# Kernel optimization log

Measured on AMD Instinct MI355X. Metric: run time of the kernel, lower is better.

Reference implementation:

```python
import jax, jax.numpy as jnp
import numpy as np


def blockdiag_matmul(x, w):
    """Block-diagonal (Monarch) linear: w has shape (nblocks, out_blk, in_blk);
    x has shape (..., nblocks*in_blk); returns (..., nblocks*out_blk)."""
    nb, q, p = w.shape
    lead = x.shape[:-1]
    xb = x.reshape(-1, nb, p)  # (tokens, nblocks, in_blk)
    out = jnp.einsum('bnp,nqp->bnq', xb, w)  # per-block matmul
    return out.reshape(*lead, nb * q)


def setup_inputs() -> dict:
    key = jax.random.key(0)
    k_x, k1, k2, k3 = jax.random.split(key, 4)
    B, S, D = 4, 4096, 2048
    NB, FF = 4, 8192  # nblocks, adjusted intermediate size
    # Kaiming-uniform-like scale for block weights (fan_in = D or FF per block-row)
    s1 = 1.0 / np.sqrt(D)
    s2 = 1.0 / np.sqrt(FF)
    return {
        'x': jax.random.normal(k_x, (B, S, D), dtype=jnp.float32),
        'w1': jax.random.normal(k1, (NB, FF // NB, D // NB), dtype=jnp.float32) * s1,
        'w3': jax.random.normal(k3, (NB, FF // NB, D // NB), dtype=jnp.float32) * s1,
        'w2': jax.random.normal(k2, (NB, D // NB, FF // NB), dtype=jnp.float32) * s2,
    }


def reference(x, w1, w3, w2):
    # SwiGLU MLP: w2(silu(w1(x)) * w3(x)), all projections block-diagonal
    gate = jax.nn.silu(blockdiag_matmul(x, w1))
    up = blockdiag_matmul(x, w3)
    return blockdiag_matmul(gate * up, w2)
```

## Files before the change

### kernel.cpp

```cpp
#include <hip/hip_runtime.h>
#include <cstdint>

typedef __attribute__((ext_vector_type(8))) short bf16x8;
typedef __attribute__((ext_vector_type(4))) float f32x4;
typedef unsigned short u16;

#define RD(p) (*(const bf16x8*)(p))

__device__ inline u16 f2bf(float f) {
  union { float f; unsigned int u; } v; v.f = f;
  unsigned int u = v.u;
  unsigned int r = (u + 0x7fffu + ((u >> 16) & 1u)) >> 16;
  return (u16)r;
}

__device__ inline void gload_lds16(const u16* g, u16* l) {
  __builtin_amdgcn_global_load_lds(
      (const __attribute__((address_space(1))) void*)g,
      (__attribute__((address_space(3))) void*)l, 16, 0, 0);
}

#define PH_BEGIN() \
  __builtin_amdgcn_s_barrier(); \
  asm volatile("s_waitcnt lgkmcnt(0)" ::: "memory"); \
  __builtin_amdgcn_s_setprio(1)
#define PH_END() \
  __builtin_amdgcn_s_setprio(0); \
  __builtin_amdgcn_s_barrier()

__global__ void cvt_all(const float* __restrict__ x, const float* __restrict__ w1,
                        const float* __restrict__ w3, const float* __restrict__ w2,
                        u16* __restrict__ xb, u16* __restrict__ w1b,
                        u16* __restrict__ w3b, u16* __restrict__ w2b) {
  const int nx = 4194304;
  const int nw = 524288;
  const int total = nx + 3 * nw;
  int stride = gridDim.x * blockDim.x;
  for (int i = blockIdx.x * blockDim.x + threadIdx.x; i < total; i += stride) {
    const float* src; u16* dst; int j;
    if (i < nx) { src = x; dst = xb; j = i; }
    else {
      int t = i - nx; int seg = t / nw; j = t - seg * nw;
      src = (seg == 0) ? w1 : (seg == 1) ? w3 : w2;
      dst = (seg == 0) ? w1b : (seg == 1) ? w3b : w2b;
    }
    const float4* s = (const float4*)(src + (size_t)j * 8);
    float4 a = s[0], b = s[1];
    union { u16 h[8]; uint4 v; } o;
    o.h[0] = f2bf(a.x); o.h[1] = f2bf(a.y); o.h[2] = f2bf(a.z); o.h[3] = f2bf(a.w);
    o.h[4] = f2bf(b.x); o.h[5] = f2bf(b.y); o.h[6] = f2bf(b.z); o.h[7] = f2bf(b.w);
    *(uint4*)(dst + (size_t)j * 8) = o.v;
  }
}

__launch_bounds__(512, 2)
__global__ void gemm_gateup2(const u16* __restrict__ xb, const u16* __restrict__ w1b,
                             const u16* __restrict__ w3b, u16* __restrict__ hout) {
  constexpr int NT = 8;
  constexpr int TPB = 8;
  constexpr int TOT = NT * TPB;
  __shared__ __attribute__((aligned(16))) u16 lA[2][256 * 64];
  __shared__ __attribute__((aligned(16))) u16 lB[2][2][128 * 64];

  int bid = blockIdx.x;
  int sw = (bid & 7) * 64 + (bid >> 3);
  int nblk = sw >> 7;
  int rem = sw & 127;
  int mt = rem >> 1, ntg = rem & 1;

  int tid = threadIdx.x, w = tid >> 6, ln = tid & 63;
  int wr = w >> 1, wc = w & 1;
  int l15 = ln & 15, l4 = ln >> 4;
  int lr = ln >> 3, ln8 = ln & 7;

  int cx0 = ((l4 ^ (l15 & 7)) << 4);
  int cx1 = (((4 + l4) ^ (l15 & 7)) << 4);
  int aOff0 = (wr * 64 + l15) * 128 + cx0;
  int aOff1 = (wr * 64 + l15) * 128 + cx1;
  int bOff0 = (wc * 64 + l15) * 128 + cx0;
  int bOff1 = (wc * 64 + l15) * 128 + cx1;

  int u0t = w * 8, u1t = 64 + w * 8;
  int rbA0 = ((u0t >> 5) << 6) + (u0t & 31);
  int rbA1 = ((u1t >> 5) << 6) + (u1t & 31);
  int dA0 = rbA0 * 128, dA1 = rbA1 * 128;
  int dB0 = u0t * 128, dB1 = u1t * 128;
  int gaA0 = rbA0 * 2048, gaA1 = rbA1 * 2048;
  int gaB0 = u0t * 512, gaB1 = u1t * 512;
  int swzg = (ln8 ^ lr) << 3;

  const u16* gA  = xb  + (size_t)(mt * 256) * 2048 + nblk * 512 + lr * 2048 + swzg;
  const u16* gB1 = w1b + (size_t)nblk * (2048 * 512) + (size_t)(ntg * 1024) * 512 + lr * 512 + swzg;
  const u16* gB3 = w3b + (size_t)nblk * (2048 * 512) + (size_t)(ntg * 1024) * 512 + lr * 512 + swzg;

  #define OFFA(s) (((s) & 7) * 64)
  #define OFFB(s) ((((s) >> 3) << 16) + (((s) & 7) * 64))

  f32x4 acc1[4][4], acc3[4][4];
#pragma unroll
  for (int i = 0; i < 4; i++)
#pragma unroll
    for (int j = 0; j < 4; j++) {
      acc1[i][j] = (f32x4){0.f, 0.f, 0.f, 0.f};
      acc3[i][j] = (f32x4){0.f, 0.f, 0.f, 0.f};
    }

  gload_lds16(gA + gaA0,          (u16*)((char*)lA + dA0));
  gload_lds16(gA + gaA1,          (u16*)((char*)lA + dA1));
  gload_lds16(gA + gaA0 + 65536,  (u16*)((char*)lA + dA0 + 4096));
  gload_lds16(gA + gaA1 + 65536,  (u16*)((char*)lA + dA1 + 4096));
  gload_lds16(gB1 + gaB0,         (u16*)((char*)lB + dB0));
  gload_lds16(gB1 + gaB1,         (u16*)((char*)lB + dB1));
  gload_lds16(gB3 + gaB0,         (u16*)((char*)lB + 16384 + dB0));
  gload_lds16(gB3 + gaB1,         (u16*)((char*)lB + 16384 + dB1));
  gload_lds16(gA + OFFA(1) + gaA0,         (u16*)((char*)lA + 32768 + dA0));
  gload_lds16(gA + OFFA(1) + gaA1,         (u16*)((char*)lA + 32768 + dA1));
  gload_lds16(gA + OFFA(1) + gaA0 + 65536, (u16*)((char*)lA + 32768 + dA0 + 4096));
  gload_lds16(gA + OFFA(1) + gaA1 + 65536, (u16*)((char*)lA + 32768 + dA1 + 4096));
  asm volatile("s_waitcnt vmcnt(4)" ::: "memory");
  __builtin_amdgcn_s_barrier();

  int sCur = 0, sNxt = 32768;
  bf16x8 aT[4][2], bb[4][2];

  for (int kt = 0; kt < TOT; ++kt) {
    const char* pA0 = (const char*)lA + (sCur + aOff0);
    const char* pA1 = (const char*)lA + (sCur + aOff1);
    const char* pB0 = (const char*)lB + (sCur + bOff0);
    const char* pB1p = (const char*)lB + (sCur + bOff1);
    int s1 = kt + 1, s2 = kt + 2;
    int oA2 = OFFA(s2), oBn = OFFB(s1);
    bool q1 = (s1 < TOT), q2 = (s2 < TOT);

#pragma unroll
    for (int f = 0; f < 2; ++f) {
      aT[f][0] = RD(pA0 + f * 2048);        aT[f][1] = RD(pA1 + f * 2048);
      aT[2 + f][0] = RD(pA0 + 4096 + f * 2048); aT[2 + f][1] = RD(pA1 + 4096 + f * 2048);
    }
#pragma unroll
    for (int g = 0; g < 4; ++g) {
      bb[g][0] = RD(pB0 + g * 2048); bb[g][1] = RD(pB1p + g * 2048);
    }
    if (q1) {
      gload_lds16(gB1 + oBn + gaB0, (u16*)((char*)lB + sNxt + dB0));
      gload_lds16(gB1 + oBn + gaB1, (u16*)((char*)lB + sNxt + dB1));
      gload_lds16(gB3 + oBn + gaB0, (u16*)((char*)lB + sNxt + 16384 + dB0));
      gload_lds16(gB3 + oBn + gaB1, (u16*)((char*)lB + sNxt + 16384 + dB1));
    }
    PH_BEGIN();
#pragma unroll
    for (int f = 0; f < 4; ++f)
#pragma unroll
      for (int g = 0; g < 4; ++g)
#pragma unroll
        for (int ks = 0; ks < 2; ++ks)
          acc1[f][g] = __builtin_amdgcn_mfma_f32_16x16x32_bf16(bb[g][ks], aT[f][ks], acc1[f][g], 0, 0, 0);
    PH_END();

#pragma unroll
    for (int g = 0; g < 4; ++g) {
      bb[g][0] = RD(pB0 + 16384 + g * 2048); bb[g][1] = RD(pB1p + 16384 + g * 2048);
    }
    if (q2) {
      gload_lds16(gA + oA2 + gaA0,         (u16*)((char*)lA + sCur + dA0));
      gload_lds16(gA + oA2 + gaA1,         (u16*)((char*)lA + sCur + dA1));
      gload_lds16(gA + oA2 + gaA0 + 65536, (u16*)((char*)lA + sCur + dA0 + 4096));
      gload_lds16(gA + oA2 + gaA1 + 65536, (u16*)((char*)lA + sCur + dA1 + 4096));
    }
    PH_BEGIN();
#pragma unroll
    for (int f = 0; f < 4; ++f)
#pragma unroll
      for (int g = 0; g < 4; ++g)
#pragma unroll
        for (int ks = 0; ks < 2; ++ks)
          acc3[f][g] = __builtin_amdgcn_mfma_f32_16x16x32_bf16(bb[g][ks], aT[f][ks], acc3[f][g], 0, 0, 0);
    __builtin_amdgcn_s_setprio(0);
    if (kt < TOT - 2)       asm volatile("s_waitcnt vmcnt(4)" ::: "memory");
    else if (kt == TOT - 2) asm volatile("s_waitcnt vmcnt(0)" ::: "memory");
    __builtin_amdgcn_s_barrier();
    sCur ^= 32768; sNxt ^= 32768;

    if ((kt & 7) == 7) {
      int nt = ntg * 8 + (kt >> 3);
      u16* Hb = hout + (size_t)(mt * 256 + wr * 64) * 8192 + nblk * 2048 + nt * 128 + wc * 64;
#pragma unroll
      for (int f = 0; f < 4; ++f) {
        u16* Hrow = Hb + (size_t)(f * 16 + l15) * 8192 + l4 * 4;
#pragma unroll
        for (int g = 0; g < 4; ++g) {
          union { u16 h[4]; uint2 v; } o;
#pragma unroll
          for (int r = 0; r < 4; ++r) {
            float gate = acc1[f][g][r];
            float up = acc3[f][g][r];
            float s = gate * __builtin_amdgcn_rcpf(1.f + __expf(-gate));
            o.h[r] = f2bf(s * up);
          }
          *(uint2*)(Hrow + g * 16) = o.v;
        }
      }
#pragma unroll
      for (int i = 0; i < 4; i++)
#pragma unroll
        for (int j = 0; j < 4; j++) {
          acc1[i][j] = (f32x4){0.f, 0.f, 0.f, 0.f};
          acc3[i][j] = (f32x4){0.f, 0.f, 0.f, 0.f};
        }
    }
  }
  #undef OFFA
  #undef OFFB
}

__launch_bounds__(512, 2)
__global__ void gemm_down2(const u16* __restrict__ hmat, const u16* __restrict__ w2b,
                           float* __restrict__ out) {
  constexpr int NT = 32;
  __shared__ __attribute__((aligned(16))) u16 lA[2][256 * 64];
  __shared__ __attribute__((aligned(16))) u16 lB[2][256 * 64];

  int bid = blockIdx.x;
  int sw = (bid & 7) * 64 + (bid >> 3);
  int nblk = sw >> 7;
  int rem = sw & 127;
  int mt = rem >> 1, nt = rem & 1;

  int tid = threadIdx.x, w = tid >> 6, ln = tid & 63;
  int mi = w >> 2, nj = w & 3;
  int l15 = ln & 15, l4 = ln >> 4;
  int lr = ln >> 3, ln8 = ln & 7;

  int cx0 = ((l4 ^ (l15 & 7)) << 4);
  int cx1 = (((4 + l4) ^ (l15 & 7)) << 4);
  int aOff0 = (mi * 128 + l15) * 128 + cx0;
  int aOff1 = (mi * 128 + l15) * 128 + cx1;
  int bOff0 = (nj * 64 + l15) * 128 + cx0;
  int bOff1 = (nj * 64 + l15) * 128 + cx1;

  int u0t = w * 8, u1t = 64 + w * 8;
  int dA0 = u0t * 128, dA1 = (64 + u1t) * 128;
  int rbB0 = ((u0t >> 5) << 6) + (u0t & 31);
  int rbB1 = ((u1t >> 5) << 6) + (u1t & 31);
  int dB0 = rbB0 * 128, dB1 = rbB1 * 128;
  int gaA0 = u0t * 8192, gaA1 = (64 + u1t) * 8192;
  int gaB0 = rbB0 * 2048, gaB1 = rbB1 * 2048;
  int swzg = (ln8 ^ lr) << 3;

  const u16* gA = hmat + (size_t)(mt * 256) * 8192 + nblk * 2048 + lr * 8192 + swzg;
  const u16* gB = w2b + (size_t)nblk * (512 * 2048) + (size_t)(nt * 256) * 2048 + lr * 2048 + swzg;

  f32x4 acc[8][4];
#pragma unroll
  for (int i = 0; i < 8; i++)
#pragma unroll
    for (int j = 0; j < 4; j++) acc[i][j] = (f32x4){0.f, 0.f, 0.f, 0.f};

  gload_lds16(gA + gaA0,            (u16*)((char*)lA + dA0));
  gload_lds16(gA + gaA1,            (u16*)((char*)lA + dA1));
  gload_lds16(gA + gaA0 + 524288,   (u16*)((char*)lA + dA0 + 8192));
  gload_lds16(gA + gaA1 + 524288,   (u16*)((char*)lA + dA1 + 8192));
  gload_lds16(gB + gaB0,            (u16*)((char*)lB + dB0));
  gload_lds16(gB + gaB1,            (u16*)((char*)lB + dB1));
  gload_lds16(gB + gaB0 + 65536,    (u16*)((char*)lB + dB0 + 4096));
  gload_lds16(gB + gaB1 + 65536,    (u16*)((char*)lB + dB1 + 4096));
  gload_lds16(gA + 64 + gaA0,           (u16*)((char*)lA + 32768 + dA0));
  gload_lds16(gA + 64 + gaA1,           (u16*)((char*)lA + 32768 + dA1));
  gload_lds16(gB + 64 + gaB0 + 65536,   (u16*)((char*)lB + 32768 + dB0 + 4096));
  gload_lds16(gB + 64 + gaB1 + 65536,   (u16*)((char*)lB + 32768 + dB1 + 4096));
  asm volatile("s_waitcnt vmcnt(4)" ::: "memory");
  __builtin_amdgcn_s_barrier();

  int sCur = 0, sNxt = 32768;
  bf16x8 aF[4][2], bLo[2][2], bHi[2][2];

  for (int kt = 0; kt < NT; ++kt) {
    const char* pA0 = (const char*)lA + (sCur + aOff0);
    const char* pA1 = (const char*)lA + (sCur + aOff1);
    const char* pB0 = (const char*)lB + (sCur + bOff0);
    const char* pB1p = (const char*)lB + (sCur + bOff1);
    int kO1 = (kt + 1) * 64, kO2 = (kt + 2) * 64;
    bool q1 = (kt + 1 < NT), q2 = (kt + 2 < NT);

#pragma unroll
    for (int f = 0; f < 4; ++f) {
      aF[f][0] = RD(pA0 + f * 2048); aF[f][1] = RD(pA1 + f * 2048);
    }
#pragma unroll
    for (int g = 0; g < 2; ++g) {
      bLo[g][0] = RD(pB0 + g * 2048);        bLo[g][1] = RD(pB1p + g * 2048);
      bHi[g][0] = RD(pB0 + 4096 + g * 2048); bHi[g][1] = RD(pB1p + 4096 + g * 2048);
    }
    if (q1) {
      gload_lds16(gB + kO1 + gaB0,          (u16*)((char*)lB + sNxt + dB0));
      gload_lds16(gB + kO1 + gaB1,          (u16*)((char*)lB + sNxt + dB1));
      gload_lds16(gA + kO1 + gaA0 + 524288, (u16*)((char*)lA + sNxt + dA0 + 8192));
      gload_lds16(gA + kO1 + gaA1 + 524288, (u16*)((char*)lA + sNxt + dA1 + 8192));
    }
    PH_BEGIN();
#pragma unroll
    for (int f = 0; f < 4; ++f)
#pragma unroll
      for (int g = 0; g < 2; ++g)
#pragma unroll
        for (int ks = 0; ks < 2; ++ks) {
          acc[f][g]     = __builtin_amdgcn_mfma_f32_16x16x32_bf16(bLo[g][ks], aF[f][ks], acc[f][g], 0, 0, 0);
          acc[f][2 + g] = __builtin_amdgcn_mfma_f32_16x16x32_bf16(bHi[g][ks], aF[f][ks], acc[f][2 + g], 0, 0, 0);
        }
    PH_END();

#pragma unroll
    for (int f = 0; f < 4; ++f) {
      aF[f][0] = RD(pA0 + 8192 + f * 2048); aF[f][1] = RD(pA1 + 8192 + f * 2048);
    }
    if (q2) {
      gload_lds16(gA + kO2 + gaA0,         (u16*)((char*)lA + sCur + dA0));
      gload_lds16(gA + kO2 + gaA1,         (u16*)((char*)lA + sCur + dA1));
      gload_lds16(gB + kO2 + gaB0 + 65536, (u16*)((char*)lB + sCur + dB0 + 4096));
      gload_lds16(gB + kO2 + gaB1 + 65536, (u16*)((char*)lB + sCur + dB1 + 4096));
    }
    PH_BEGIN();
#pragma unroll
    for (int f = 0; f < 4; ++f)
#pragma unroll
      for (int g = 0; g < 2; ++g)
#pragma unroll
        for (int ks = 0; ks < 2; ++ks) {
          acc[4 + f][g]     = __builtin_amdgcn_mfma_f32_16x16x32_bf16(bLo[g][ks], aF[f][ks], acc[4 + f][g], 0, 0, 0);
          acc[4 + f][2 + g] = __builtin_amdgcn_mfma_f32_16x16x32_bf16(bHi[g][ks], aF[f][ks], acc[4 + f][2 + g], 0, 0, 0);
        }
    __builtin_amdgcn_s_setprio(0);
    if (kt < NT - 2)       asm volatile("s_waitcnt vmcnt(4)" ::: "memory");
    else if (kt == NT - 2) asm volatile("s_waitcnt vmcnt(0)" ::: "memory");
    __builtin_amdgcn_s_barrier();
    sCur ^= 32768; sNxt ^= 32768;
  }

  float* Ob = out + (size_t)(mt * 256 + mi * 128) * 2048 + nblk * 512 + nt * 256 + nj * 64;
#pragma unroll
  for (int f = 0; f < 8; ++f) {
    float* Orow = Ob + (size_t)(f * 16 + l15) * 2048 + l4 * 4;
#pragma unroll
    for (int g = 0; g < 4; ++g)
      *(f32x4*)(Orow + g * 16) = acc[f][g];
  }
}

extern "C" void kernel_launch(void* const* d_in, const int* in_sizes, int n_in,
                              void* d_out, int out_size, void* d_ws, size_t ws_size,
                              hipStream_t stream) {
  const float* x  = (const float*)d_in[0];
  const float* w1 = (const float*)d_in[1];
  const float* w3 = (const float*)d_in[2];
  const float* w2 = (const float*)d_in[3];

  char* ws = (char*)d_ws;
  u16* xb  = (u16*)(ws);
  u16* w1b = (u16*)(ws + 67108864);
  u16* w3b = (u16*)(ws + 75497472);
  u16* w2b = (u16*)(ws + 83886080);
  u16* h   = (u16*)(ws + 92274688);

  cvt_all<<<2048, 256, 0, stream>>>(x, w1, w3, w2, xb, w1b, w3b, w2b);

  gemm_gateup2<<<512, 512, 0, stream>>>(xb, w1b, w3b, h);
  gemm_down2<<<512, 512, 0, stream>>>(h, w2b, (float*)d_out);
}
```

Baseline: 500.5 us.

## Load gate/up A operand directly into registers and halve N-tiles per block

The gate/up GEMM now loads the activation (A) fragments straight from global memory into registers with double buffering, instead of staging them through LDS. Only the weight tiles still go through LDS. Each block now covers 4 N-tiles instead of 8, and the grid doubles to 1024 blocks. The goal is to free LDS capacity and bandwidth and add parallelism, at the cost of more register pressure, less coalesced direct global reads, and re-reading A across twice as many blocks.

Result: slower. 595.2 us (+18.9%).

```diff
diff --git a/kernel.cpp b/kernel.cpp
--- a/kernel.cpp
+++ b/kernel.cpp
@@ -54,19 +54,18 @@
 }
 
 __launch_bounds__(512, 2)
-__global__ void gemm_gateup2(const u16* __restrict__ xb, const u16* __restrict__ w1b,
-                             const u16* __restrict__ w3b, u16* __restrict__ hout) {
+__global__ void gemm_gateup_ar(const u16* __restrict__ xb, const u16* __restrict__ w1b,
+                               const u16* __restrict__ w3b, u16* __restrict__ hout) {
   constexpr int NT = 8;
-  constexpr int TPB = 8;
+  constexpr int TPB = 4;
   constexpr int TOT = NT * TPB;
-  __shared__ __attribute__((aligned(16))) u16 lA[2][256 * 64];
   __shared__ __attribute__((aligned(16))) u16 lB[2][2][128 * 64];
 
   int bid = blockIdx.x;
-  int sw = (bid & 7) * 64 + (bid >> 3);
-  int nblk = sw >> 7;
-  int rem = sw & 127;
-  int mt = rem >> 1, ntg = rem & 1;
+  int sw = (bid & 7) * 128 + (bid >> 3);
+  int nblk = sw >> 8;
+  int rem = sw & 255;
+  int mt = rem >> 2, ntg = rem & 3;
 
   int tid = threadIdx.x, w = tid >> 6, ln = tid & 63;
   int wr = w >> 1, wc = w & 1;
@@ -75,23 +74,18 @@
 
   int cx0 = ((l4 ^ (l15 & 7)) << 4);
   int cx1 = (((4 + l4) ^ (l15 & 7)) << 4);
-  int aOff0 = (wr * 64 + l15) * 128 + cx0;
-  int aOff1 = (wr * 64 + l15) * 128 + cx1;
   int bOff0 = (wc * 64 + l15) * 128 + cx0;
   int bOff1 = (wc * 64 + l15) * 128 + cx1;
 
   int u0t = w * 8, u1t = 64 + w * 8;
-  int rbA0 = ((u0t >> 5) << 6) + (u0t & 31);
-  int rbA1 = ((u1t >> 5) << 6) + (u1t & 31);
-  int dA0 = rbA0 * 128, dA1 = rbA1 * 128;
   int dB0 = u0t * 128, dB1 = u1t * 128;
-  int gaA0 = rbA0 * 2048, gaA1 = rbA1 * 2048;
   int gaB0 = u0t * 512, gaB1 = u1t * 512;
   int swzg = (ln8 ^ lr) << 3;
 
-  const u16* gA  = xb  + (size_t)(mt * 256) * 2048 + nblk * 512 + lr * 2048 + swzg;
-  const u16* gB1 = w1b + (size_t)nblk * (2048 * 512) + (size_t)(ntg * 1024) * 512 + lr * 512 + swzg;
-  const u16* gB3 = w3b + (size_t)nblk * (2048 * 512) + (size_t)(ntg * 1024) * 512 + lr * 512 + swzg;
+  const u16* gB1 = w1b + (size_t)nblk * (2048 * 512) + (size_t)(ntg * 512) * 512 + lr * 512 + swzg;
+  const u16* gB3 = w3b + (size_t)nblk * (2048 * 512) + (size_t)(ntg * 512) * 512 + lr * 512 + swzg;
+
+  const u16* gAr = xb + (size_t)(mt * 256 + wr * 64 + l15) * 2048 + nblk * 512 + l4 * 8;
 
   #define OFFA(s) (((s) & 7) * 64)
   #define OFFB(s) ((((s) >> 3) << 16) + (((s) & 7) * 64))
@@ -105,110 +99,118 @@
       acc3[i][j] = (f32x4){0.f, 0.f, 0.f, 0.f};
     }
 
-  gload_lds16(gA + gaA0,          (u16*)((char*)lA + dA0));
-  gload_lds16(gA + gaA1,          (u16*)((char*)lA + dA1));
-  gload_lds16(gA + gaA0 + 65536,  (u16*)((char*)lA + dA0 + 4096));
-  gload_lds16(gA + gaA1 + 65536,  (u16*)((char*)lA + dA1 + 4096));
-  gload_lds16(gB1 + gaB0,         (u16*)((char*)lB + dB0));
-  gload_lds16(gB1 + gaB1,         (u16*)((char*)lB + dB1));
-  gload_lds16(gB3 + gaB0,         (u16*)((char*)lB + 16384 + dB0));
-  gload_lds16(gB3 + gaB1,         (u16*)((char*)lB + 16384 + dB1));
-  gload_lds16(gA + OFFA(1) + gaA0,         (u16*)((char*)lA + 32768 + dA0));
-  gload_lds16(gA + OFFA(1) + gaA1,         (u16*)((char*)lA + 32768 + dA1));
-  gload_lds16(gA + OFFA(1) + gaA0 + 65536, (u16*)((char*)lA + 32768 + dA0 + 4096));
-  gload_lds16(gA + OFFA(1) + gaA1 + 65536, (u16*)((char*)lA + 32768 + dA1 + 4096));
-  asm volatile("s_waitcnt vmcnt(4)" ::: "memory");
+  bf16x8 aA[4][2], aB[4][2], bb[4][2];
+
+  gload_lds16(gB1 + gaB0, (u16*)((char*)lB + dB0));
+  gload_lds16(gB1 + gaB1, (u16*)((char*)lB + dB1));
+  gload_lds16(gB3 + gaB0, (u16*)((char*)lB + 16384 + dB0));
+  gload_lds16(gB3 + gaB1, (u16*)((char*)lB + 16384 + dB1));
+#pragma unroll
+  for (int f = 0; f < 4; ++f) {
+    aA[f][0] = *(const bf16x8*)(gAr + f * 32768);
+    aA[f][1] = *(const bf16x8*)(gAr + f * 32768 + 32);
+  }
+  asm volatile("s_waitcnt vmcnt(8)" ::: "memory");
   __builtin_amdgcn_s_barrier();
 
   int sCur = 0, sNxt = 32768;
-  bf16x8 aT[4][2], bb[4][2];
-
-  for (int kt = 0; kt < TOT; ++kt) {
-    const char* pA0 = (const char*)lA + (sCur + aOff0);
-    const char* pA1 = (const char*)lA + (sCur + aOff1);
-    const char* pB0 = (const char*)lB + (sCur + bOff0);
-    const char* pB1p = (const char*)lB + (sCur + bOff1);
-    int s1 = kt + 1, s2 = kt + 2;
-    int oA2 = OFFA(s2), oBn = OFFB(s1);
-    bool q1 = (s1 < TOT), q2 = (s2 < TOT);
-
-#pragma unroll
-    for (int f = 0; f < 2; ++f) {
-      aT[f][0] = RD(pA0 + f * 2048);        aT[f][1] = RD(pA1 + f * 2048);
-      aT[2 + f][0] = RD(pA0 + 4096 + f * 2048); aT[2 + f][1] = RD(pA1 + 4096 + f * 2048);
-    }
-#pragma unroll
-    for (int g = 0; g < 4; ++g) {
-      bb[g][0] = RD(pB0 + g * 2048); bb[g][1] = RD(pB1p + g * 2048);
-    }
-    if (q1) {
-      gload_lds16(gB1 + oBn + gaB0, (u16*)((char*)lB + sNxt + dB0));
-      gload_lds16(gB1 + oBn + gaB1, (u16*)((char*)lB + sNxt + dB1));
-      gload_lds16(gB3 + oBn + gaB0, (u16*)((char*)lB + sNxt + 16384 + dB0));
-      gload_lds16(gB3 + oBn + gaB1, (u16*)((char*)lB + sNxt + 16384 + dB1));
-    }
-    PH_BEGIN();
-#pragma unroll
-    for (int f = 0; f < 4; ++f)
-#pragma unroll
-      for (int g = 0; g < 4; ++g)
-#pragma unroll
-        for (int ks = 0; ks < 2; ++ks)
-          acc1[f][g] = __builtin_amdgcn_mfma_f32_16x16x32_bf16(bb[g][ks], aT[f][ks], acc1[f][g], 0, 0, 0);
-    PH_END();
-
-#pragma unroll
-    for (int g = 0; g < 4; ++g) {
-      bb[g][0] = RD(pB0 + 16384 + g * 2048); bb[g][1] = RD(pB1p + 16384 + g * 2048);
-    }
-    if (q2) {
-      gload_lds16(gA + oA2 + gaA0,         (u16*)((char*)lA + sCur + dA0));
-      gload_lds16(gA + oA2 + gaA1,         (u16*)((char*)lA + sCur + dA1));
-      gload_lds16(gA + oA2 + gaA0 + 65536, (u16*)((char*)lA + sCur + dA0 + 4096));
-      gload_lds16(gA + oA2 + gaA1 + 65536, (u16*)((char*)lA + sCur + dA1 + 4096));
-    }
-    PH_BEGIN();
-#pragma unroll
-    for (int f = 0; f < 4; ++f)
-#pragma unroll
-      for (int g = 0; g < 4; ++g)
-#pragma unroll
-        for (int ks = 0; ks < 2; ++ks)
-          acc3[f][g] = __builtin_amdgcn_mfma_f32_16x16x32_bf16(bb[g][ks], aT[f][ks], acc3[f][g], 0, 0, 0);
-    __builtin_amdgcn_s_setprio(0);
-    if (kt < TOT - 2)       asm volatile("s_waitcnt vmcnt(4)" ::: "memory");
-    else if (kt == TOT - 2) asm volatile("s_waitcnt vmcnt(0)" ::: "memory");
-    __builtin_amdgcn_s_barrier();
-    sCur ^= 32768; sNxt ^= 32768;
-
-    if ((kt & 7) == 7) {
-      int nt = ntg * 8 + (kt >> 3);
-      u16* Hb = hout + (size_t)(mt * 256 + wr * 64) * 8192 + nblk * 2048 + nt * 128 + wc * 64;
-#pragma unroll
-      for (int f = 0; f < 4; ++f) {
-        u16* Hrow = Hb + (size_t)(f * 16 + l15) * 8192 + l4 * 4;
-#pragma unroll
-        for (int g = 0; g < 4; ++g) {
-          union { u16 h[4]; uint2 v; } o;
-#pragma unroll
-          for (int r = 0; r < 4; ++r) {
-            float gate = acc1[f][g][r];
-            float up = acc3[f][g][r];
-            float s = gate * __builtin_amdgcn_rcpf(1.f + __expf(-gate));
-            o.h[r] = f2bf(s * up);
-          }
-          *(uint2*)(Hrow + g * 16) = o.v;
-        }
-      }
-#pragma unroll
-      for (int i = 0; i < 4; i++)
-#pragma unroll
-        for (int j = 0; j < 4; j++) {
-          acc1[i][j] = (f32x4){0.f, 0.f, 0.f, 0.f};
-          acc3[i][j] = (f32x4){0.f, 0.f, 0.f, 0.f};
-        }
-    }
-  }
+
+  #define GUP_STEP(AC, AN, KT, LAST)                                              \
+  {                                                                               \
+    const int kt_ = (KT);                                                         \
+    const char* pB0 = (const char*)lB + (sCur + bOff0);                           \
+    const char* pB1p = (const char*)lB + (sCur + bOff1);                          \
+    int s1_ = kt_ + 1;                                                            \
+    bool q1_ = (s1_ < TOT);                                                       \
+    int oBn_ = OFFB(s1_), oAn_ = OFFA(s1_);                                       \
+                            \
+    _Pragma("unroll")                                                             \
+    for (int g = 0; g < 4; ++g) {                                                 \
+      bb[g][0] = RD(pB0 + g * 2048); bb[g][1] = RD(pB1p + g * 2048);              \
+    }                                                                             \
+    if (q1_) {                                                                    \
+      gload_lds16(gB1 + oBn_ + gaB0, (u16*)((char*)lB + sNxt + dB0));             \
+      gload_lds16(gB1 + oBn_ + gaB1, (u16*)((char*)lB + sNxt + dB1));             \
+      gload_lds16(gB3 + oBn_ + gaB0, (u16*)((char*)lB + sNxt + 16384 + dB0));     \
+      gload_lds16(gB3 + oBn_ + gaB1, (u16*)((char*)lB + sNxt + 16384 + dB1));     \
+    }                                                                             \
+    __builtin_amdgcn_s_barrier();                                                 \
+    if (LAST) asm volatile("s_waitcnt lgkmcnt(0) vmcnt(0)" ::: "memory");         \
+    else      asm volatile("s_waitcnt lgkmcnt(0) vmcnt(4)" ::: "memory");         \
+    __builtin_amdgcn_s_setprio(1);                                                \
+    _Pragma("unroll")                                                             \
+    for (int f = 0; f < 4; ++f)                                                   \
+      _Pragma("unroll")                                                           \
+      for (int g = 0; g < 4; ++g)                                                 \
+        _Pragma("unroll")                                                         \
+        for (int ks = 0; ks < 2; ++ks)                                            \
+          acc1[f][g] = __builtin_amdgcn_mfma_f32_16x16x32_bf16(bb[g][ks], AC[f][ks], acc1[f][g], 0, 0, 0); \
+    __builtin_amdgcn_s_setprio(0);                                                \
+    __builtin_amdgcn_s_barrier();                                                 \
+                                        \
+    _Pragma("unroll")                                                             \
+    for (int g = 0; g < 4; ++g) {                                                 \
+      bb[g][0] = RD(pB0 + 16384 + g * 2048); bb[g][1] = RD(pB1p + 16384 + g * 2048); \
+    }                                                                             \
+    if (q1_) {                                                                    \
+      _Pragma("unroll")                                                           \
+      for (int f = 0; f < 4; ++f) {                                               \
+        AN[f][0] = *(const bf16x8*)(gAr + oAn_ + f * 32768);                      \
+        AN[f][1] = *(const bf16x8*)(gAr + oAn_ + f * 32768 + 32);                 \
+      }                                                                           \
+    }                                                                             \
+    __builtin_amdgcn_s_barrier();                                                 \
+    asm volatile("s_waitcnt lgkmcnt(0)" ::: "memory");                            \
+    __builtin_amdgcn_s_setprio(1);                                                \
+    _Pragma("unroll")                                                             \
+    for (int f = 0; f < 4; ++f)                                                   \
+      _Pragma("unroll")                                                           \
+      for (int g = 0; g < 4; ++g)                                                 \
+        _Pragma("unroll")                                                         \
+        for (int ks = 0; ks < 2; ++ks)                                            \
+          acc3[f][g] = __builtin_amdgcn_mfma_f32_16x16x32_bf16(bb[g][ks], AC[f][ks], acc3[f][g], 0, 0, 0); \
+    __builtin_amdgcn_s_setprio(0);                                                \
+    if (LAST) asm volatile("s_waitcnt vmcnt(0)" ::: "memory");                    \
+    else      asm volatile("s_waitcnt vmcnt(8)" ::: "memory");                    \
+    __builtin_amdgcn_s_barrier();                                                 \
+    sCur ^= 32768; sNxt ^= 32768;                                                 \
+    if ((kt_ & 7) == 7) {                                                         \
+      int nt_ = ntg * 4 + (kt_ >> 3);                                             \
+      u16* Hb = hout + (size_t)(mt * 256 + wr * 64) * 8192 + nblk * 2048 + nt_ * 128 + wc * 64; \
+      _Pragma("unroll")                                                           \
+      for (int f = 0; f < 4; ++f) {                                               \
+        u16* Hrow = Hb + (size_t)(f * 16 + l15) * 8192 + l4 * 4;                  \
+        _Pragma("unroll")                                                         \
+        for (int g = 0; g < 4; ++g) {                                             \
+          union { u16 h[4]; uint2 v; } o;                                         \
+          _Pragma("unroll")                                                       \
+          for (int r = 0; r < 4; ++r) {                                           \
+            float gate = acc1[f][g][r];                                           \
+            float up = acc3[f][g][r];                                             \
+            float s = gate * __builtin_amdgcn_rcpf(1.f + __expf(-gate));          \
+            o.h[r] = f2bf(s * up);                                                \
+          }                                                                       \
+          *(uint2*)(Hrow + g * 16) = o.v;                                         \
+        }                                                                         \
+      }                                                                           \
+      _Pragma("unroll")                                                           \
+      for (int i = 0; i < 4; i++)                                                 \
+        _Pragma("unroll")                                                         \
+        for (int j = 0; j < 4; j++) {                                             \
+          acc1[i][j] = (f32x4){0.f, 0.f, 0.f, 0.f};                               \
+          acc3[i][j] = (f32x4){0.f, 0.f, 0.f, 0.f};                               \
+        }                                                                         \
+    }                                                                             \
+  }
+
+  for (int kt = 0; kt < TOT - 2; kt += 2) {
+    GUP_STEP(aA, aB, kt, false);
+    GUP_STEP(aB, aA, kt + 1, false);
+  }
+  GUP_STEP(aA, aB, TOT - 2, false);
+  GUP_STEP(aB, aA, TOT - 1, true);
+
+  #undef GUP_STEP
   #undef OFFA
   #undef OFFB
 }
@@ -363,6 +365,6 @@
 
   cvt_all<<<2048, 256, 0, stream>>>(x, w1, w3, w2, xb, w1b, w3b, w2b);
 
-  gemm_gateup2<<<512, 512, 0, stream>>>(xb, w1b, w3b, h);
+  gemm_gateup_ar<<<1024, 512, 0, stream>>>(xb, w1b, w3b, h);
   gemm_down2<<<512, 512, 0, stream>>>(h, w2b, (float*)d_out);
 }
```
